# Performance work log

Measured on AMD Instinct MI355X. Metric: run time of the kernel, lower is better.

The kernel has to match this reference:

```python
import jax, jax.numpy as jnp
import numpy as np

N = 50000
E = 800000
HID = 128
OUT = 64
HEADS = 4
NEG_SLOPE = 0.2


def gat_layer(x, edge_index, W, att_src, att_dst, bias):
    """PyG-style GATConv: shared linear for src/dst, additive attention,
    self-loops, segment softmax over incoming edges, concat heads + bias."""
    n = x.shape[0]
    H, C = att_src.shape
    # add self loops (PyG default add_self_loops=True)
    loops = jnp.arange(n, dtype=edge_index.dtype)
    src = jnp.concatenate([edge_index[0], loops])  # message sources j
    dst = jnp.concatenate([edge_index[1], loops])  # aggregation targets i
    xl = (x @ W).reshape(n, H, C)                  # [N,H,C]
    a_s = jnp.einsum('nhc,hc->nh', xl, att_src)    # [N,H]
    a_d = jnp.einsum('nhc,hc->nh', xl, att_dst)    # [N,H]
    e = jax.nn.leaky_relu(a_s[src] + a_d[dst], NEG_SLOPE)   # [E',H]
    m = jax.ops.segment_max(e, dst, num_segments=n)         # stable softmax
    e = jnp.exp(e - m[dst])
    denom = jax.ops.segment_sum(e, dst, num_segments=n)
    alpha = e / (denom[dst] + 1e-16)                        # [E',H]
    msg = xl[src] * alpha[:, :, None]                       # [E',H,C]
    out = jax.ops.segment_sum(msg, dst, num_segments=n)     # [N,H,C]
    return out.reshape(n, H * C) + bias


def setup_inputs() -> dict:
    key = jax.random.key(0)
    ks = jax.random.split(key, 16)
    C = HID // HEADS  # per-head channels = 32
    x = jax.random.normal(ks[0], (N, HID), dtype=jnp.float32)
    edge_indices = jax.random.randint(ks[1], (3, 2, E), 0, N, dtype=jnp.int32)
    s = 0.1
    inp = {
        'x': x,
        'edge_indices': edge_indices,
        'W1': jax.random.normal(ks[2], (HID, HEADS * C), dtype=jnp.float32) * s,
        'as1': jax.random.normal(ks[3], (HEADS, C), dtype=jnp.float32) * s,
        'ad1': jax.random.normal(ks[4], (HEADS, C), dtype=jnp.float32) * s,
        'b1': jnp.zeros((HEADS * C,), dtype=jnp.float32),
        'W2': jax.random.normal(ks[5], (HID, HEADS * C), dtype=jnp.float32) * s,
        'as2': jax.random.normal(ks[6], (HEADS, C), dtype=jnp.float32) * s,
        'ad2': jax.random.normal(ks[7], (HEADS, C), dtype=jnp.float32) * s,
        'b2': jnp.zeros((HEADS * C,), dtype=jnp.float32),
        'W3': jax.random.normal(ks[8], (HID, OUT), dtype=jnp.float32) * s,
        'as3': jax.random.normal(ks[9], (1, OUT), dtype=jnp.float32) * s,
        'ad3': jax.random.normal(ks[10], (1, OUT), dtype=jnp.float32) * s,
        'b3': jnp.zeros((OUT,), dtype=jnp.float32),
    }
    return inp


def reference(x, edge_indices, W1, as1, ad1, b1, W2, as2, ad2, b2, W3, as3, ad3, b3):
    h = jax.nn.relu(gat_layer(x, edge_indices[0], W1, as1, ad1, b1))
    h = jax.nn.relu(gat_layer(h, edge_indices[1], W2, as2, ad2, b2))
    out = gat_layer(h, edge_indices[2], W3, as3, ad3, b3)  # no ReLU on last layer
    return out
```

## Files before the change

### kernel.cpp

```cpp
#include <hip/hip_runtime.h>

typedef unsigned short u16;
typedef unsigned int u32;
typedef __attribute__((ext_vector_type(8))) short short8;
typedef __attribute__((ext_vector_type(4))) float f32x4;

#define HID 128

static inline int cdiv(long long a, int b) { return (int)((a + b - 1) / b); }

__device__ __forceinline__ float bfbits(u32 u) { union { u32 u; float f; } c; c.u = u; return c.f; }
__device__ __forceinline__ u16 f2bf(float f) {
  union { float f; u32 u; } c; c.f = f;
  u32 u = c.u;
  return (u16)((u + 0x7fffu + ((u >> 16) & 1u)) >> 16);
}
__device__ __forceinline__ u32 pack2bf(float a, float b) {
  return (u32)f2bf(a) | ((u32)f2bf(b) << 16);
}

__global__ __launch_bounds__(256) void prep_wt3(
    const float* __restrict__ W1, const float* __restrict__ W2,
    const float* __restrict__ W3, u16* __restrict__ wt1, u16* __restrict__ wt2,
    u16* __restrict__ wt3) {
  int y = blockIdx.y;
  const float* W = (y == 0) ? W1 : ((y == 1) ? W2 : W3);
  u16* WT = (y == 0) ? wt1 : ((y == 1) ? wt2 : wt3);
  int cout = (y == 2) ? 64 : 128;
  int idx = blockIdx.x * 256 + threadIdx.x;
  if (idx < 128 * cout) {
    int k = idx / cout, c = idx - k * cout;
    WT[c * 128 + k] = f2bf(W[idx]);
  }
}

template <int COUT, int HEADS>
__global__ __launch_bounds__(256) void gemm_attn_mfma(
    const float* __restrict__ Hin, const u16* __restrict__ WT,
    const float* __restrict__ attS, const float* __restrict__ attD,
    u16* __restrict__ XL, float* __restrict__ aS, float* __restrict__ aD, int n) {
  constexpr int NT = COUT / 16;
  constexpr int C = COUT / HEADS;
  constexpr int TPH = C / 16;

  int t = threadIdx.x;
  int wv = t >> 6, ln = t & 63;
  int lrow = ln & 15;
  int lk = ln >> 4;
  int row = blockIdx.x * 64 + wv * 16 + lrow;
  bool ok = (row < n);
  int rowc = ok ? row : (n - 1);

  const float* hp = Hin + (size_t)rowc * HID;

  float4 hv[8];
#pragma unroll
  for (int kb = 0; kb < 4; ++kb) {
    hv[2 * kb] = *(const float4*)(hp + kb * 32 + lk * 8);
    hv[2 * kb + 1] = *(const float4*)(hp + kb * 32 + lk * 8 + 4);
  }

  f32x4 acc[NT];
#pragma unroll
  for (int ct = 0; ct < NT; ++ct) acc[ct] = {0.f, 0.f, 0.f, 0.f};

#pragma unroll
  for (int kb = 0; kb < 4; ++kb) {
    union { short8 s; u32 u[4]; } bb;
    float4 h0 = hv[2 * kb], h1 = hv[2 * kb + 1];
    bb.u[0] = pack2bf(h0.x, h0.y);
    bb.u[1] = pack2bf(h0.z, h0.w);
    bb.u[2] = pack2bf(h1.x, h1.y);
    bb.u[3] = pack2bf(h1.z, h1.w);
    const u16* wp = WT + (size_t)lrow * HID + kb * 32 + lk * 8;
#pragma unroll
    for (int ct = 0; ct < NT; ++ct) {
      short8 aw = *(const short8*)(wp + (size_t)ct * 16 * HID);
      acc[ct] = __builtin_amdgcn_mfma_f32_16x16x32_bf16(aw, bb.s, acc[ct], 0, 0, 0);
    }
  }

  float pS[HEADS], pD[HEADS];
#pragma unroll
  for (int h = 0; h < HEADS; ++h) { pS[h] = 0.f; pD[h] = 0.f; }
#pragma unroll
  for (int ct = 0; ct < NT; ++ct) {
    float4 sv = *(const float4*)(attS + ct * 16 + lk * 4);
    float4 dv = *(const float4*)(attD + ct * 16 + lk * 4);
    int h = ct / TPH;
    pS[h] += acc[ct][0] * sv.x + acc[ct][1] * sv.y + acc[ct][2] * sv.z + acc[ct][3] * sv.w;
    pD[h] += acc[ct][0] * dv.x + acc[ct][1] * dv.y + acc[ct][2] * dv.z + acc[ct][3] * dv.w;
  }
#pragma unroll
  for (int h = 0; h < HEADS; ++h) {
    pS[h] += __shfl_xor(pS[h], 16);
    pS[h] += __shfl_xor(pS[h], 32);
    pD[h] += __shfl_xor(pD[h], 16);
    pD[h] += __shfl_xor(pD[h], 32);
  }
  if (lk == 0 && ok) {
    if (HEADS == 4) {
      *(float4*)(aS + (size_t)row * 4) = make_float4(pS[0], pS[1], pS[2], pS[3]);
      *(float4*)(aD + (size_t)row * 4) = make_float4(pD[0], pD[1], pD[2], pD[3]);
    } else {
      aS[row] = pS[0];
      aD[row] = pD[0];
    }
  }

  if (ok) {
    u32* Xp = (u32*)XL + (size_t)row * (COUT / 2);
#pragma unroll
    for (int ct = 0; ct < NT; ++ct) {
      *(uint2*)(Xp + ct * 8 + lk * 2) =
          make_uint2(pack2bf(acc[ct][0], acc[ct][1]), pack2bf(acc[ct][2], acc[ct][3]));
    }
  }
}

#define PSTR 16

__global__ __launch_bounds__(256) void bucket_hist(const int* __restrict__ ei,
                                                   int* __restrict__ cntP,
                                                   int e4, int rem, int E, int NB) {
  int L = blockIdx.y;
  const int* dst = ei + (size_t)(2 * L + 1) * E;
  __shared__ int cnt[256];
  int t = threadIdx.x;
  cnt[t] = 0;
  __syncthreads();
  int gbase = blockIdx.x * 1024 + t;
#pragma unroll
  for (int u = 0; u < 4; ++u) {
    int g = gbase + u * 256;
    if (g < e4) {
      int4 d = *(const int4*)(dst + g * 4);
      atomicAdd(&cnt[d.x >> 8], 1);
      atomicAdd(&cnt[d.y >> 8], 1);
      atomicAdd(&cnt[d.z >> 8], 1);
      atomicAdd(&cnt[d.w >> 8], 1);
    }
  }
  if (blockIdx.x == 0 && t < rem) atomicAdd(&cnt[dst[e4 * 4 + t] >> 8], 1);
  __syncthreads();
  int c = cnt[t];
  if (t < NB && c > 0) atomicAdd(&cntP[(L * NB + t) * PSTR], c);
}

__global__ __launch_bounds__(256) void bucket_scan(const int* __restrict__ cntP,
                                                   int* __restrict__ bucketOff,
                                                   int* __restrict__ curP, int NB, int E) {
  int L = blockIdx.x;
  int t = threadIdx.x;
  int lane = t & 63, wid = t >> 6;
  __shared__ int wpart[4];
  int v = (t < NB) ? cntP[(L * NB + t) * PSTR] : 0;
  int inc = v;
#pragma unroll
  for (int off = 1; off < 64; off <<= 1) {
    int w = __shfl_up(inc, (unsigned)off, 64);
    if (lane >= off) inc += w;
  }
  if (lane == 63) wpart[wid] = inc;
  __syncthreads();
  if (t == 0) {
    int a = 0;
#pragma unroll
    for (int k = 0; k < 4; ++k) { int tmp = wpart[k]; wpart[k] = a; a += tmp; }
  }
  __syncthreads();
  int ex = wpart[wid] + inc - v;
  if (t < NB) {
    bucketOff[L * (NB + 1) + t] = ex;
    curP[(L * NB + t) * PSTR] = ex;
  }
  if (t == 0) bucketOff[L * (NB + 1) + NB] = E;
}

__global__ __launch_bounds__(256) void bucket_scatter(const int* __restrict__ ei,
                                                      int* __restrict__ curP,
                                                      int2* __restrict__ pairsAll,
                                                      int e4, int rem, int E, int NB) {
  int L = blockIdx.y;
  const int* src = ei + (size_t)(2 * L) * E;
  const int* dst = src + E;
  int2* pairs = pairsAll + (size_t)L * E;
  __shared__ int cnt[256];
  __shared__ int baseS[256];
  int t = threadIdx.x;
  cnt[t] = 0;
  __syncthreads();

  int gbase = blockIdx.x * 1024 + t;
  int4 dv[4], sv[4];
  bool val[4];
#pragma unroll
  for (int u = 0; u < 4; ++u) {
    int g = gbase + u * 256;
    val[u] = (g < e4);
    if (val[u]) {
      dv[u] = *(const int4*)(dst + g * 4);
      sv[u] = *(const int4*)(src + g * 4);
      atomicAdd(&cnt[dv[u].x >> 8], 1);
      atomicAdd(&cnt[dv[u].y >> 8], 1);
      atomicAdd(&cnt[dv[u].z >> 8], 1);
      atomicAdd(&cnt[dv[u].w >> 8], 1);
    }
  }
  int tailS = 0, tailD = 0;
  bool hasTail = (blockIdx.x == 0 && t < rem);
  if (hasTail) {
    tailD = dst[e4 * 4 + t];
    tailS = src[e4 * 4 + t];
    atomicAdd(&cnt[tailD >> 8], 1);
  }
  __syncthreads();
  int c = cnt[t];
  if (t < NB && c > 0) baseS[t] = atomicAdd(&curP[(L * NB + t) * PSTR], c);
  __syncthreads();
  cnt[t] = 0;
  __syncthreads();
#pragma unroll
  for (int u = 0; u < 4; ++u) {
    if (val[u]) {
      int b, p;
      b = dv[u].x >> 8; p = atomicAdd(&cnt[b], 1); pairs[baseS[b] + p] = make_int2(sv[u].x, dv[u].x);
      b = dv[u].y >> 8; p = atomicAdd(&cnt[b], 1); pairs[baseS[b] + p] = make_int2(sv[u].y, dv[u].y);
      b = dv[u].z >> 8; p = atomicAdd(&cnt[b], 1); pairs[baseS[b] + p] = make_int2(sv[u].z, dv[u].z);
      b = dv[u].w >> 8; p = atomicAdd(&cnt[b], 1); pairs[baseS[b] + p] = make_int2(sv[u].w, dv[u].w);
    }
  }
  if (hasTail) {
    int b = tailD >> 8;
    int p = atomicAdd(&cnt[b], 1);
    pairs[baseS[b] + p] = make_int2(tailS, tailD);
  }
}

__global__ __launch_bounds__(256) void csr_finalize(const int2* __restrict__ pairsAll,
                                                    const int* __restrict__ bucketOff,
                                                    int* __restrict__ indptrAll,
                                                    int* __restrict__ srcIdxAll,
                                                    int N, int E, int NB) {
  int L = blockIdx.y, b = blockIdx.x;
  const int2* pairs = pairsAll + (size_t)L * E;
  int* indptr = indptrAll + (size_t)L * (N + 1);
  int* srcL = srcIdxAll + (size_t)L * (E + N);
  int base = b << 8;
  int nodes = min(256, N - base);
  int p0 = bucketOff[L * (NB + 1) + b];
  int p1 = bucketOff[L * (NB + 1) + b + 1];

  __shared__ int cnt[256];
  __shared__ int wpart[4];
  int t = threadIdx.x;
  int lane = t & 63, wid = t >> 6;
  cnt[t] = 0;
  __syncthreads();

  for (int i = p0 + t; i < p1; i += 256) atomicAdd(&cnt[pairs[i].y - base], 1);
  __syncthreads();

  int v = (t < nodes) ? cnt[t] + 1 : 0;
  int inc = v;
#pragma unroll
  for (int off = 1; off < 64; off <<= 1) {
    int w = __shfl_up(inc, (unsigned)off, 64);
    if (lane >= off) inc += w;
  }
  if (lane == 63) wpart[wid] = inc;
  __syncthreads();
  if (t == 0) {
    int a = 0;
#pragma unroll
    for (int k = 0; k < 4; ++k) { int tmp = wpart[k]; wpart[k] = a; a += tmp; }
  }
  __syncthreads();
  int ex = wpart[wid] + inc - v;
  __syncthreads();
  if (t < nodes) {
    int segStart = p0 + base + ex;
    indptr[base + t] = segStart;
    srcL[segStart] = base + t;
    cnt[t] = segStart + 1;
  }
  if (b == NB - 1 && t == 0) indptr[N] = E + N;
  __syncthreads();

  for (int i = p0 + t; i < p1; i += 256) {
    int2 pr = pairs[i];
    int p = atomicAdd(&cnt[pr.y - base], 1);
    srcL[p] = pr.x;
  }
}

template <int COUT, int HEADS, bool RELU>
__global__ __launch_bounds__(256) void aggregate(
    const u16* __restrict__ XL, const float* __restrict__ aS, const float* __restrict__ aD,
    const int* __restrict__ indptr, const int* __restrict__ srcIdx,
    const float* __restrict__ bias, float* __restrict__ outF, int n) {
  constexpr int LPG = 8;
  constexpr int G = 8;
  constexpr int VPL = COUT / LPG;
  constexpr int U32PL = VPL / 2;
  constexpr int C = COUT / HEADS;
  int wave = (blockIdx.x * blockDim.x + threadIdx.x) >> 6;
  if (wave >= n) return;
  int lane = threadIdx.x & 63;
  int g = lane >> 3;
  int cl = lane & 7;
  int col0 = cl * VPL;
  int h = col0 / C;
  int i = wave;
  float ad = aD[(size_t)i * HEADS + h];
  int e0 = indptr[i], e1 = indptr[i + 1];
  int deg = e1 - e0;
  int jreg = srcIdx[e0 + min(lane, deg - 1)];

  float s = 0.f;
  float acc[VPL];
#pragma unroll
  for (int v = 0; v < VPL; ++v) acc[v] = 0.f;
  const u32* XL32 = (const u32*)XL;

  auto fetch = [&](int b, float& av, uint4& q0, uint4& q1, bool& act) {
    int k0 = b * G + g;
    act = (k0 < deg);
    int k = act ? k0 : 0;
    int js = __shfl(jreg, min(k, 63));
    if (k >= 64) js = srcIdx[e0 + k];
    av = aS[(size_t)js * HEADS + h];
    const u32* xp = XL32 + (size_t)js * (COUT / 2) + cl * U32PL;
    q0 = *(const uint4*)xp;
    if (U32PL == 8) q1 = *(const uint4*)(xp + 4);
  };
  auto consume = [&](float av, const uint4& q0, const uint4& q1, bool act) {
    float l = av + ad;
    l = (l >= 0.f) ? l : 0.2f * l;
    float el = act ? __expf(fminf(l, 60.f)) : 0.f;
    s += el;
    acc[0] += el * bfbits(q0.x << 16);
    acc[1] += el * bfbits(q0.x & 0xffff0000u);
    acc[2] += el * bfbits(q0.y << 16);
    acc[3] += el * bfbits(q0.y & 0xffff0000u);
    acc[4] += el * bfbits(q0.z << 16);
    acc[5] += el * bfbits(q0.z & 0xffff0000u);
    acc[6] += el * bfbits(q0.w << 16);
    acc[7] += el * bfbits(q0.w & 0xffff0000u);
    if (U32PL == 8) {
      acc[VPL - 8] += el * bfbits(q1.x << 16);
      acc[VPL - 7] += el * bfbits(q1.x & 0xffff0000u);
      acc[VPL - 6] += el * bfbits(q1.y << 16);
      acc[VPL - 5] += el * bfbits(q1.y & 0xffff0000u);
      acc[VPL - 4] += el * bfbits(q1.z << 16);
      acc[VPL - 3] += el * bfbits(q1.z & 0xffff0000u);
      acc[VPL - 2] += el * bfbits(q1.w << 16);
      acc[VPL - 1] += el * bfbits(q1.w & 0xffff0000u);
    }
  };

  int nb = (deg + G - 1) / G;
  float aa, ab;
  uint4 pa0 = make_uint4(0, 0, 0, 0), pa1 = pa0, pb0 = pa0, pb1 = pa0;
  bool acta, actb;
  fetch(0, aa, pa0, pa1, acta);
  for (int b = 0; b < nb; b += 2) {
    if (b + 1 < nb) {
      fetch(b + 1, ab, pb0, pb1, actb);
      consume(aa, pa0, pa1, acta);
      if (b + 2 < nb) fetch(b + 2, aa, pa0, pa1, acta);
      consume(ab, pb0, pb1, actb);
    } else {
      consume(aa, pa0, pa1, acta);
    }
  }

#pragma unroll
  for (int mk = LPG; mk < 64; mk <<= 1) {
    s += __shfl_xor(s, mk);
#pragma unroll
    for (int v = 0; v < VPL; ++v) acc[v] += __shfl_xor(acc[v], mk);
  }

  if (g == 0) {
    float inv = 1.f / (s + 1e-16f);
    float o[VPL];
#pragma unroll
    for (int v = 0; v < VPL; ++v) {
      o[v] = acc[v] * inv + bias[col0 + v];
      if (RELU) o[v] = fmaxf(o[v], 0.f);
    }
    float* op = outF + (size_t)i * COUT + col0;
#pragma unroll
    for (int v4 = 0; v4 < VPL / 4; ++v4)
      *(float4*)(op + v4 * 4) = make_float4(o[v4 * 4], o[v4 * 4 + 1], o[v4 * 4 + 2], o[v4 * 4 + 3]);
  }
}

extern "C" void kernel_launch(void* const* d_in, const int* in_sizes, int n_in,
                              void* d_out, int out_size, void* d_ws, size_t ws_size,
                              hipStream_t stream) {
  const float* x = (const float*)d_in[0];
  const int* ei = (const int*)d_in[1];
  const float* W1 = (const float*)d_in[2];
  const float* as1 = (const float*)d_in[3];
  const float* ad1 = (const float*)d_in[4];
  const float* b1 = (const float*)d_in[5];
  const float* W2 = (const float*)d_in[6];
  const float* as2 = (const float*)d_in[7];
  const float* ad2 = (const float*)d_in[8];
  const float* b2 = (const float*)d_in[9];
  const float* W3 = (const float*)d_in[10];
  const float* as3 = (const float*)d_in[11];
  const float* ad3 = (const float*)d_in[12];
  const float* b3 = (const float*)d_in[13];

  int N = in_sizes[0] / HID;
  int E = in_sizes[1] / 6;
  int NB = cdiv(N, 256);

  char* w = (char*)d_ws;
  auto alloc = [&](size_t bytes) {
    void* q = (void*)w;
    w += (bytes + 255) & ~(size_t)255;
    return q;
  };
  float* bufH = (float*)alloc((size_t)N * HID * 4);
  u16* bufXL = (u16*)alloc((size_t)N * HID * 2);
  float* aS = (float*)alloc((size_t)N * 4 * 4);
  float* aD = (float*)alloc((size_t)N * 4 * 4);
  u16* wt1 = (u16*)alloc((size_t)128 * 128 * 2);
  u16* wt2 = (u16*)alloc((size_t)128 * 128 * 2);
  u16* wt3 = (u16*)alloc((size_t)64 * 128 * 2);
  int* cntP = (int*)alloc((size_t)3 * NB * PSTR * 4);
  int* curP = (int*)alloc((size_t)3 * NB * PSTR * 4);
  int* bucketOff = (int*)alloc((size_t)3 * (NB + 1) * 4);
  int2* pairsAll = (int2*)alloc((size_t)3 * E * 8);
  int* indptrAll = (int*)alloc((size_t)3 * (N + 1) * 4);
  int* srcIdxAll = (int*)alloc((size_t)3 * (E + N) * 4);

  int e4 = E >> 2, rem = E & 3;
  int gx = cdiv(e4, 1024);

  {
    dim3 g(64, 3);
    prep_wt3<<<g, 256, 0, stream>>>(W1, W2, W3, wt1, wt2, wt3);
  }

  hipMemsetAsync(cntP, 0, (size_t)3 * NB * PSTR * 4, stream);
  {
    dim3 g(gx, 3);
    bucket_hist<<<g, 256, 0, stream>>>(ei, cntP, e4, rem, E, NB);
  }
  bucket_scan<<<3, 256, 0, stream>>>(cntP, bucketOff, curP, NB, E);
  {
    dim3 g(gx, 3);
    bucket_scatter<<<g, 256, 0, stream>>>(ei, curP, pairsAll, e4, rem, E, NB);
  }
  {
    dim3 g(NB, 3);
    csr_finalize<<<g, 256, 0, stream>>>(pairsAll, bucketOff, indptrAll, srcIdxAll, N, E, NB);
  }

  gemm_attn_mfma<128, 4><<<cdiv(N, 64), 256, 0, stream>>>(x, wt1, as1, ad1, bufXL, aS, aD, N);
  aggregate<128, 4, true><<<cdiv(N, 4), 256, 0, stream>>>(
      bufXL, aS, aD, indptrAll, srcIdxAll, b1, bufH, N);
  gemm_attn_mfma<128, 4><<<cdiv(N, 64), 256, 0, stream>>>(bufH, wt2, as2, ad2, bufXL, aS, aD, N);
  aggregate<128, 4, true><<<cdiv(N, 4), 256, 0, stream>>>(
      bufXL, aS, aD, indptrAll + (N + 1), srcIdxAll + (size_t)(E + N), b2, bufH, N);
  gemm_attn_mfma<64, 1><<<cdiv(N, 64), 256, 0, stream>>>(bufH, wt3, as3, ad3, bufXL, aS, aD, N);
  aggregate<64, 1, false><<<cdiv(N, 4), 256, 0, stream>>>(
      bufXL, aS, aD, indptrAll + 2 * (N + 1), srcIdxAll + (size_t)2 * (E + N), b3,
      (float*)d_out, N);
}
```

Baseline: 317.2 us.

## Store hidden activations as bf16, restructure aggregation to node-per-lane-group, fuse weight prep

Hidden activations between layers are now written as bf16 by the aggregation kernel and read directly by the GEMM. This halves intermediate traffic and removes the float-to-bf16 conversion in the GEMM. The aggregation kernel now assigns 16 or 8 lanes per node (4 or 8 nodes per wave), each lane handling 8 columns. It walks edges serially with one-ahead prefetching, which drops the cross-group shuffle reductions but creates lane divergence from uneven degrees. Weight transposition is folded into the histogram kernel as an extra grid row, saving one launch.

```diff
diff --git a/kernel.cpp b/kernel.cpp
--- a/kernel.cpp
+++ b/kernel.cpp
@@ -19,24 +19,9 @@
   return (u32)f2bf(a) | ((u32)f2bf(b) << 16);
 }
 
-__global__ __launch_bounds__(256) void prep_wt3(
-    const float* __restrict__ W1, const float* __restrict__ W2,
-    const float* __restrict__ W3, u16* __restrict__ wt1, u16* __restrict__ wt2,
-    u16* __restrict__ wt3) {
-  int y = blockIdx.y;
-  const float* W = (y == 0) ? W1 : ((y == 1) ? W2 : W3);
-  u16* WT = (y == 0) ? wt1 : ((y == 1) ? wt2 : wt3);
-  int cout = (y == 2) ? 64 : 128;
-  int idx = blockIdx.x * 256 + threadIdx.x;
-  if (idx < 128 * cout) {
-    int k = idx / cout, c = idx - k * cout;
-    WT[c * 128 + k] = f2bf(W[idx]);
-  }
-}
-
-template <int COUT, int HEADS>
+template <int COUT, int HEADS, bool BF16IN>
 __global__ __launch_bounds__(256) void gemm_attn_mfma(
-    const float* __restrict__ Hin, const u16* __restrict__ WT,
+    const void* __restrict__ HinV, const u16* __restrict__ WT,
     const float* __restrict__ attS, const float* __restrict__ attD,
     u16* __restrict__ XL, float* __restrict__ aS, float* __restrict__ aD, int n) {
   constexpr int NT = COUT / 16;
@@ -51,32 +36,43 @@
   bool ok = (row < n);
   int rowc = ok ? row : (n - 1);
 
-  const float* hp = Hin + (size_t)rowc * HID;
-
-  float4 hv[8];
+  short8 bb[4];
+  if (BF16IN) {
+    const u16* hp = (const u16*)HinV + (size_t)rowc * HID;
+#pragma unroll
+    for (int kb = 0; kb < 4; ++kb)
+      bb[kb] = *(const short8*)(hp + kb * 32 + lk * 8);
+  } else {
+    const float* hp = (const float*)HinV + (size_t)rowc * HID;
+    float4 hv[8];
+#pragma unroll
+    for (int kb = 0; kb < 4; ++kb) {
+      hv[2 * kb] = *(const float4*)(hp + kb * 32 + lk * 8);
+      hv[2 * kb + 1] = *(const float4*)(hp + kb * 32 + lk * 8 + 4);
+    }
+#pragma unroll
+    for (int kb = 0; kb < 4; ++kb) {
+      union { short8 s; u32 u[4]; } pk;
+      float4 h0 = hv[2 * kb], h1 = hv[2 * kb + 1];
+      pk.u[0] = pack2bf(h0.x, h0.y);
+      pk.u[1] = pack2bf(h0.z, h0.w);
+      pk.u[2] = pack2bf(h1.x, h1.y);
+      pk.u[3] = pack2bf(h1.z, h1.w);
+      bb[kb] = pk.s;
+    }
+  }
+
+  f32x4 acc[NT];
+#pragma unroll
+  for (int ct = 0; ct < NT; ++ct) acc[ct] = {0.f, 0.f, 0.f, 0.f};
+
 #pragma unroll
   for (int kb = 0; kb < 4; ++kb) {
-    hv[2 * kb] = *(const float4*)(hp + kb * 32 + lk * 8);
-    hv[2 * kb + 1] = *(const float4*)(hp + kb * 32 + lk * 8 + 4);
-  }
-
-  f32x4 acc[NT];
-#pragma unroll
-  for (int ct = 0; ct < NT; ++ct) acc[ct] = {0.f, 0.f, 0.f, 0.f};
-
-#pragma unroll
-  for (int kb = 0; kb < 4; ++kb) {
-    union { short8 s; u32 u[4]; } bb;
-    float4 h0 = hv[2 * kb], h1 = hv[2 * kb + 1];
-    bb.u[0] = pack2bf(h0.x, h0.y);
-    bb.u[1] = pack2bf(h0.z, h0.w);
-    bb.u[2] = pack2bf(h1.x, h1.y);
-    bb.u[3] = pack2bf(h1.z, h1.w);
     const u16* wp = WT + (size_t)lrow * HID + kb * 32 + lk * 8;
 #pragma unroll
     for (int ct = 0; ct < NT; ++ct) {
       short8 aw = *(const short8*)(wp + (size_t)ct * 16 * HID);
-      acc[ct] = __builtin_amdgcn_mfma_f32_16x16x32_bf16(aw, bb.s, acc[ct], 0, 0, 0);
+      acc[ct] = __builtin_amdgcn_mfma_f32_16x16x32_bf16(aw, bb[kb], acc[ct], 0, 0, 0);
     }
   }
 
@@ -120,9 +116,26 @@
 
 #define PSTR 16
 
-__global__ __launch_bounds__(256) void bucket_hist(const int* __restrict__ ei,
-                                                   int* __restrict__ cntP,
-                                                   int e4, int rem, int E, int NB) {
+__global__ __launch_bounds__(256) void bucket_hist_prep(
+    const int* __restrict__ ei, int* __restrict__ cntP, int e4, int rem, int E, int NB,
+    const float* __restrict__ W1, const float* __restrict__ W2,
+    const float* __restrict__ W3, u16* __restrict__ wt1, u16* __restrict__ wt2,
+    u16* __restrict__ wt3) {
+  if (blockIdx.y == 3) {
+    int bx = blockIdx.x;
+    if (bx >= 160) return;
+    int y = (bx >= 128) ? 2 : (bx >= 64 ? 1 : 0);
+    int b0 = (y == 0) ? 0 : ((y == 1) ? 64 : 128);
+    const float* W = (y == 0) ? W1 : ((y == 1) ? W2 : W3);
+    u16* WT = (y == 0) ? wt1 : ((y == 1) ? wt2 : wt3);
+    int cout = (y == 2) ? 64 : 128;
+    int idx = (bx - b0) * 256 + threadIdx.x;
+    if (idx < 128 * cout) {
+      int k = idx / cout, c = idx - k * cout;
+      WT[c * 128 + k] = f2bf(W[idx]);
+    }
+    return;
+  }
   int L = blockIdx.y;
   const int* dst = ei + (size_t)(2 * L + 1) * E;
   __shared__ int cnt[256];
@@ -294,106 +307,78 @@
   }
 }
 
-template <int COUT, int HEADS, bool RELU>
+template <int COUT, int HEADS, bool RELU, bool OUTBF>
 __global__ __launch_bounds__(256) void aggregate(
     const u16* __restrict__ XL, const float* __restrict__ aS, const float* __restrict__ aD,
     const int* __restrict__ indptr, const int* __restrict__ srcIdx,
-    const float* __restrict__ bias, float* __restrict__ outF, int n) {
-  constexpr int LPG = 8;
-  constexpr int G = 8;
-  constexpr int VPL = COUT / LPG;
-  constexpr int U32PL = VPL / 2;
+    const float* __restrict__ bias, void* __restrict__ outV, int n) {
+  constexpr int LPN = COUT / 8;
+  constexpr int NPW = 64 / LPN;
   constexpr int C = COUT / HEADS;
-  int wave = (blockIdx.x * blockDim.x + threadIdx.x) >> 6;
-  if (wave >= n) return;
+
+  int wid = (blockIdx.x * blockDim.x + threadIdx.x) >> 6;
   int lane = threadIdx.x & 63;
-  int g = lane >> 3;
-  int cl = lane & 7;
-  int col0 = cl * VPL;
+  int sub = lane / LPN;
+  int cl = lane % LPN;
+  int i = wid * NPW + sub;
+  bool ok = (i < n);
+  int ic = ok ? i : (n - 1);
+
+  int col0 = cl * 8;
   int h = col0 / C;
-  int i = wave;
-  float ad = aD[(size_t)i * HEADS + h];
-  int e0 = indptr[i], e1 = indptr[i + 1];
+  float ad = aD[(size_t)ic * HEADS + h];
+  int e0 = indptr[ic], e1 = indptr[ic + 1];
   int deg = e1 - e0;
-  int jreg = srcIdx[e0 + min(lane, deg - 1)];
-
+
+  const u32* XL32 = (const u32*)XL;
   float s = 0.f;
-  float acc[VPL];
-#pragma unroll
-  for (int v = 0; v < VPL; ++v) acc[v] = 0.f;
-  const u32* XL32 = (const u32*)XL;
-
-  auto fetch = [&](int b, float& av, uint4& q0, uint4& q1, bool& act) {
-    int k0 = b * G + g;
-    act = (k0 < deg);
-    int k = act ? k0 : 0;
-    int js = __shfl(jreg, min(k, 63));
-    if (k >= 64) js = srcIdx[e0 + k];
-    av = aS[(size_t)js * HEADS + h];
-    const u32* xp = XL32 + (size_t)js * (COUT / 2) + cl * U32PL;
-    q0 = *(const uint4*)xp;
-    if (U32PL == 8) q1 = *(const uint4*)(xp + 4);
-  };
-  auto consume = [&](float av, const uint4& q0, const uint4& q1, bool act) {
-    float l = av + ad;
+  float acc[8];
+#pragma unroll
+  for (int v = 0; v < 8; ++v) acc[v] = 0.f;
+
+  int jn = srcIdx[e0];
+  float an = aS[(size_t)jn * HEADS + h];
+  uint4 qn = *(const uint4*)(XL32 + (size_t)jn * (COUT / 2) + cl * 4);
+
+#pragma unroll 2
+  for (int k = 0; k < deg; ++k) {
+    float ac = an;
+    uint4 qc = qn;
+    if (k + 1 < deg) {
+      int j2 = srcIdx[e0 + k + 1];
+      an = aS[(size_t)j2 * HEADS + h];
+      qn = *(const uint4*)(XL32 + (size_t)j2 * (COUT / 2) + cl * 4);
+    }
+    float l = ac + ad;
     l = (l >= 0.f) ? l : 0.2f * l;
-    float el = act ? __expf(fminf(l, 60.f)) : 0.f;
+    float el = __expf(fminf(l, 60.f));
     s += el;
-    acc[0] += el * bfbits(q0.x << 16);
-    acc[1] += el * bfbits(q0.x & 0xffff0000u);
-    acc[2] += el * bfbits(q0.y << 16);
-    acc[3] += el * bfbits(q0.y & 0xffff0000u);
-    acc[4] += el * bfbits(q0.z << 16);
-    acc[5] += el * bfbits(q0.z & 0xffff0000u);
-    acc[6] += el * bfbits(q0.w << 16);
-    acc[7] += el * bfbits(q0.w & 0xffff0000u);
-    if (U32PL == 8) {
-      acc[VPL - 8] += el * bfbits(q1.x << 16);
-      acc[VPL - 7] += el * bfbits(q1.x & 0xffff0000u);
-      acc[VPL - 6] += el * bfbits(q1.y << 16);
-      acc[VPL - 5] += el * bfbits(q1.y & 0xffff0000u);
-      acc[VPL - 4] += el * bfbits(q1.z << 16);
-      acc[VPL - 3] += el * bfbits(q1.z & 0xffff0000u);
-      acc[VPL - 2] += el * bfbits(q1.w << 16);
-      acc[VPL - 1] += el * bfbits(q1.w & 0xffff0000u);
-    }
-  };
-
-  int nb = (deg + G - 1) / G;
-  float aa, ab;
-  uint4 pa0 = make_uint4(0, 0, 0, 0), pa1 = pa0, pb0 = pa0, pb1 = pa0;
-  bool acta, actb;
-  fetch(0, aa, pa0, pa1, acta);
-  for (int b = 0; b < nb; b += 2) {
-    if (b + 1 < nb) {
-      fetch(b + 1, ab, pb0, pb1, actb);
-      consume(aa, pa0, pa1, acta);
-      if (b + 2 < nb) fetch(b + 2, aa, pa0, pa1, acta);
-      consume(ab, pb0, pb1, actb);
-    } else {
-      consume(aa, pa0, pa1, acta);
-    }
-  }
-
-#pragma unroll
-  for (int mk = LPG; mk < 64; mk <<= 1) {
-    s += __shfl_xor(s, mk);
-#pragma unroll
-    for (int v = 0; v < VPL; ++v) acc[v] += __shfl_xor(acc[v], mk);
-  }
-
-  if (g == 0) {
-    float inv = 1.f / (s + 1e-16f);
-    float o[VPL];
-#pragma unroll
-    for (int v = 0; v < VPL; ++v) {
-      o[v] = acc[v] * inv + bias[col0 + v];
-      if (RELU) o[v] = fmaxf(o[v], 0.f);
-    }
-    float* op = outF + (size_t)i * COUT + col0;
-#pragma unroll
-    for (int v4 = 0; v4 < VPL / 4; ++v4)
-      *(float4*)(op + v4 * 4) = make_float4(o[v4 * 4], o[v4 * 4 + 1], o[v4 * 4 + 2], o[v4 * 4 + 3]);
+    acc[0] += el * bfbits(qc.x << 16);
+    acc[1] += el * bfbits(qc.x & 0xffff0000u);
+    acc[2] += el * bfbits(qc.y << 16);
+    acc[3] += el * bfbits(qc.y & 0xffff0000u);
+    acc[4] += el * bfbits(qc.z << 16);
+    acc[5] += el * bfbits(qc.z & 0xffff0000u);
+    acc[6] += el * bfbits(qc.w << 16);
+    acc[7] += el * bfbits(qc.w & 0xffff0000u);
+  }
+
+  if (!ok) return;
+  float inv = 1.f / (s + 1e-16f);
+  float o[8];
+#pragma unroll
+  for (int v = 0; v < 8; ++v) {
+    o[v] = acc[v] * inv + bias[col0 + v];
+    if (RELU) o[v] = fmaxf(o[v], 0.f);
+  }
+  if (OUTBF) {
+    u32* op = (u32*)outV + (size_t)i * (COUT / 2) + cl * 4;
+    *(uint4*)op = make_uint4(pack2bf(o[0], o[1]), pack2bf(o[2], o[3]),
+                             pack2bf(o[4], o[5]), pack2bf(o[6], o[7]));
+  } else {
+    float* op = (float*)outV + (size_t)i * COUT + col0;
+    *(float4*)op = make_float4(o[0], o[1], o[2], o[3]);
+    *(float4*)(op + 4) = make_float4(o[4], o[5], o[6], o[7]);
   }
 }
 
@@ -425,7 +410,7 @@
     w += (bytes + 255) & ~(size_t)255;
     return q;
   };
-  float* bufH = (float*)alloc((size_t)N * HID * 4);
+  u16* bufH = (u16*)alloc((size_t)N * HID * 2);
   u16* bufXL = (u16*)alloc((size_t)N * HID * 2);
   float* aS = (float*)alloc((size_t)N * 4 * 4);
   float* aD = (float*)alloc((size_t)N * 4 * 4);
@@ -441,16 +426,13 @@
 
   int e4 = E >> 2, rem = E & 3;
   int gx = cdiv(e4, 1024);
-
-  {
-    dim3 g(64, 3);
-    prep_wt3<<<g, 256, 0, stream>>>(W1, W2, W3, wt1, wt2, wt3);
-  }
+  int gxh = (gx > 160) ? gx : 160;
 
   hipMemsetAsync(cntP, 0, (size_t)3 * NB * PSTR * 4, stream);
   {
-    dim3 g(gx, 3);
-    bucket_hist<<<g, 256, 0, stream>>>(ei, cntP, e4, rem, E, NB);
+    dim3 g(gxh, 4);
+    bucket_hist_prep<<<g, 256, 0, stream>>>(ei, cntP, e4, rem, E, NB,
+                                            W1, W2, W3, wt1, wt2, wt3);
   }
   bucket_scan<<<3, 256, 0, stream>>>(cntP, bucketOff, curP, NB, E);
   {
@@ -462,14 +444,17 @@
     csr_finalize<<<g, 256, 0, stream>>>(pairsAll, bucketOff, indptrAll, srcIdxAll, N, E, NB);
   }
 
-  gemm_attn_mfma<128, 4><<<cdiv(N, 64), 256, 0, stream>>>(x, wt1, as1, ad1, bufXL, aS, aD, N);
-  aggregate<128, 4, true><<<cdiv(N, 4), 256, 0, stream>>>(
+  gemm_attn_mfma<128, 4, false><<<cdiv(N, 64), 256, 0, stream>>>(
+      x, wt1, as1, ad1, bufXL, aS, aD, N);
+  aggregate<128, 4, true, true><<<cdiv(N, 16), 256, 0, stream>>>(
       bufXL, aS, aD, indptrAll, srcIdxAll, b1, bufH, N);
-  gemm_attn_mfma<128, 4><<<cdiv(N, 64), 256, 0, stream>>>(bufH, wt2, as2, ad2, bufXL, aS, aD, N);
-  aggregate<128, 4, true><<<cdiv(N, 4), 256, 0, stream>>>(
+  gemm_attn_mfma<128, 4, true><<<cdiv(N, 64), 256, 0, stream>>>(
+      bufH, wt2, as2, ad2, bufXL, aS, aD, N);
+  aggregate<128, 4, true, true><<<cdiv(N, 16), 256, 0, stream>>>(
       bufXL, aS, aD, indptrAll + (N + 1), srcIdxAll + (size_t)(E + N), b2, bufH, N);
-  gemm_attn_mfma<64, 1><<<cdiv(N, 64), 256, 0, stream>>>(bufH, wt3, as3, ad3, bufXL, aS, aD, N);
-  aggregate<64, 1, false><<<cdiv(N, 4), 256, 0, stream>>>(
+  gemm_attn_mfma<64, 1, true><<<cdiv(N, 64), 256, 0, stream>>>(
+      bufH, wt3, as3, ad3, bufXL, aS, aD, N);
+  aggregate<64, 1, false, false><<<cdiv(N, 32), 256, 0, stream>>>(
       bufXL, aS, aD, indptrAll + 2 * (N + 1), srcIdxAll + (size_t)2 * (E + N), b3,
-      (float*)d_out, N);
-}
+      d_out, N);
+}
```

Result: slower. 330.1 us (+4.1%).
